# Performance work log

Hardware: AMD Instinct MI355X
Metric: run time of the kernel (lower is better)

## Reference

```python
import jax, jax.numpy as jnp
import numpy as np

FP8_MAX = 448.0  # e4m3fn max
ACT_EPS = 1e-4
W_EPS = 1e-6
BLK = 128


def quant_dequant_act_1x128(x):
    # x: [E, M, K]. One scale per (row, 128-col) tile; scale = max(|x|, eps)/448.
    E, M, K = x.shape
    xb = x.reshape(E, M, K // BLK, BLK)
    amax = jnp.max(jnp.abs(xb), axis=-1, keepdims=True)
    safe = jnp.maximum(amax, ACT_EPS)
    q = (xb * (FP8_MAX / safe)).astype(jnp.float8_e4m3fn)
    return (q.astype(jnp.float32) * (safe / FP8_MAX)).reshape(E, M, K)


def quant_dequant_weight_128x128(w):
    # w: [E, N, K]. One scale per 128x128 block; scale = max(|w|, eps)/448.
    E, N, K = w.shape
    wb = w.reshape(E, N // BLK, BLK, K // BLK, BLK)
    amax = jnp.max(jnp.abs(wb), axis=(2, 4), keepdims=True)
    safe = jnp.maximum(amax, W_EPS)
    q = (wb * (FP8_MAX / safe)).astype(jnp.float8_e4m3fn)
    return (q.astype(jnp.float32) * (safe / FP8_MAX)).reshape(E, N, K)


def setup_inputs() -> dict:
    key = jax.random.key(0)
    kx, kw = jax.random.split(key)
    E, M, K, N = 8, 4096, 2048, 2048
    x = jax.random.normal(kx, (E, M, K), dtype=jnp.float32)
    weight = jax.random.normal(kw, (E, N, K), dtype=jnp.float32) * 0.02
    return {"x": x, "weight": weight}


def reference(x, weight):
    # fp8 blockwise quantize both operands, then grouped GEMM per expert.
    xq = quant_dequant_act_1x128(x)          # [E, M, K]
    wq = quant_dequant_weight_128x128(weight)  # [E, N, K]
    return jnp.einsum('emk,enk->emn', xq, wq)  # [E, M, N]
```

## Files before the change

### kernel.cpp

```cpp
#include <hip/hip_runtime.h>

typedef float f32x4 __attribute__((ext_vector_type(4)));
typedef float f32x16 __attribute__((ext_vector_type(16)));

static constexpr int E_ = 8, M_ = 4096, K_ = 2048, N_ = 2048;
static constexpr int KB_ = 16;
static constexpr int NB128 = N_ / 128;
static constexpr int BM = 256, BN = 128, BK = 128;
static constexpr int KT = K_ / BK;
static constexpr int MT2 = M_ / BM;
static constexpr int NT2 = N_ / BN;
#define FP8MAX 448.0f

__global__ __launch_bounds__(256) void quant_x_kernel(const float* __restrict__ x,
                                                      unsigned char* __restrict__ qx,
                                                      float* __restrict__ sx) {
  long tile = (long)blockIdx.x * 8 + (threadIdx.x >> 5);
  int lane = threadIdx.x & 31;
  f32x4 v = *(const f32x4*)(x + tile * 128 + lane * 4);
  float am = fmaxf(fmaxf(fabsf(v[0]), fabsf(v[1])), fmaxf(fabsf(v[2]), fabsf(v[3])));
#pragma unroll
  for (int off = 16; off; off >>= 1) am = fmaxf(am, __shfl_xor(am, off, 32));
  float safe = fmaxf(am, 1e-4f);
  float qs = FP8MAX / safe;
  int pk = 0;
  pk = __builtin_amdgcn_cvt_pk_fp8_f32(v[0] * qs, v[1] * qs, pk, false);
  pk = __builtin_amdgcn_cvt_pk_fp8_f32(v[2] * qs, v[3] * qs, pk, true);
  *(int*)(qx + tile * 128 + lane * 4) = pk;
  if (lane == 0) sx[tile] = safe / FP8MAX;
}

__global__ __launch_bounds__(256) void quant_w_kernel(const float* __restrict__ w,
                                                      unsigned char* __restrict__ qw,
                                                      float* __restrict__ sw) {
  int b = blockIdx.x;
  int kb = b % KB_;
  int t2 = b / KB_;
  int nb = t2 % NB128;
  int e = t2 / NB128;
  int tid = threadIdx.x;
  int r = tid >> 1;
  int c0 = (tid & 1) * 64;
  const float* base = w + ((long)(e * N_ + nb * 128 + r)) * K_ + kb * 128 + c0;
  f32x4 v[16];
  float am = 0.f;
#pragma unroll
  for (int j = 0; j < 16; ++j) {
    v[j] = *(const f32x4*)(base + j * 4);
    am = fmaxf(am, fmaxf(fmaxf(fabsf(v[j][0]), fabsf(v[j][1])),
                         fmaxf(fabsf(v[j][2]), fabsf(v[j][3]))));
  }
#pragma unroll
  for (int off = 32; off; off >>= 1) am = fmaxf(am, __shfl_xor(am, off, 64));
  __shared__ float red[4];
  if ((tid & 63) == 0) red[tid >> 6] = am;
  __syncthreads();
  am = fmaxf(fmaxf(red[0], red[1]), fmaxf(red[2], red[3]));
  float safe = fmaxf(am, 1e-6f);
  float qs = FP8MAX / safe;
  unsigned char* outp = qw + ((long)(e * N_ + nb * 128 + r)) * K_ + kb * 128 + c0;
#pragma unroll
  for (int j4 = 0; j4 < 4; ++j4) {
    uint4 pkv;
    unsigned int* pp = (unsigned int*)&pkv;
#pragma unroll
    for (int q = 0; q < 4; ++q) {
      int j = j4 * 4 + q;
      int pk = 0;
      pk = __builtin_amdgcn_cvt_pk_fp8_f32(v[j][0] * qs, v[j][1] * qs, pk, false);
      pk = __builtin_amdgcn_cvt_pk_fp8_f32(v[j][2] * qs, v[j][3] * qs, pk, true);
      pp[q] = (unsigned int)pk;
    }
    *(uint4*)(outp + j4 * 16) = pkv;
  }
  if (tid == 0) sw[(e * NB128 + nb) * KB_ + kb] = safe / FP8MAX;
}

__device__ inline void gload16(const void* g, void* l) {
  __builtin_amdgcn_global_load_lds(
      (const __attribute__((address_space(1))) unsigned int*)g,
      (__attribute__((address_space(3))) unsigned int*)l, 16, 0, 0);
}

#define BAR __builtin_amdgcn_s_barrier()

#define MMACC(ACC, AV, BV, SXV)                                                 \
  do {                                                                          \
    f32x16 p = {0.f, 0.f, 0.f, 0.f, 0.f, 0.f, 0.f, 0.f,                        \
                0.f, 0.f, 0.f, 0.f, 0.f, 0.f, 0.f, 0.f};                        \
    __builtin_amdgcn_s_setprio(1);                                              \
    _Pragma("unroll") for (int ks = 0; ks < 8; ++ks)                            \
        p = __builtin_amdgcn_mfma_f32_32x32x16_fp8_fp8(AV[ks], BV[ks], p, 0, 0, 0); \
    __builtin_amdgcn_s_setprio(0);                                              \
    ACC += p * (SXV);                                                           \
  } while (0)

#define LDSX(SV, MB)                                                            \
  do {                                                                          \
    _Pragma("unroll") for (int g = 0; g < 4; ++g) {                             \
      f32x4 t = *(const f32x4*)&sxl[kt][wr * 64 + (MB) * 32 + hi * 4 + g * 8];  \
      _Pragma("unroll") for (int j = 0; j < 4; ++j) SV[g * 4 + j] = t[j] * swk; \
    }                                                                           \
  } while (0)

__global__ __launch_bounds__(512, 2) void gemm_kernel(
    const unsigned char* __restrict__ qx, const unsigned char* __restrict__ qw,
    const float* __restrict__ sx, const float* __restrict__ sw,
    float* __restrict__ out) {
  __shared__ unsigned char As[2][BM * BK];
  __shared__ unsigned char Bs[2][BN * BK];
  __shared__ float sxl[KT][BM];
  __shared__ float swl[KT];

  const int e = blockIdx.y;
  const int x = blockIdx.x;
  const int swz = (x & 7) * 32 + (x >> 3);
  const int mt = swz >> 4, nt = swz & 15;
  const int brow = mt * BM, bcol = nt * BN;

  const int tid = threadIdx.x;
  const int w = tid >> 6, l = tid & 63;
  const int wr = w >> 1, wc = w & 1;
  const int r32 = l & 31, hi = l >> 5, rx = l & 7;

  const unsigned char* Ab = qx + (size_t)(e * M_ + brow) * K_;
  const unsigned char* Bb = qw + (size_t)(e * N_ + bcol) * K_;

  {
    int row = tid >> 1, h = (tid & 1) * 8;
    const float* sp = sx + (size_t)(e * M_ + brow + row) * KB_ + h;
    f32x4 s0 = *(const f32x4*)sp;
    f32x4 s1 = *(const f32x4*)(sp + 4);
#pragma unroll
    for (int j = 0; j < 4; ++j) {
      sxl[h + j][row] = s0[j];
      sxl[h + 4 + j][row] = s1[j];
    }
    if (tid < KT) swl[tid] = sw[(e * NB128 + nt) * KB_ + tid];
  }
  __syncthreads();

  const int c8 = l & 7, r8 = (l >> 3) & 7;
  const int srcswz = (c8 ^ r8) * 16;
  auto stageA = [&](int rowbase, int kt2, int tb) {
    gload16(Ab + (size_t)(rowbase + w * 8 + (l >> 3)) * K_ + kt2 * BK + srcswz,
            &As[tb][(rowbase + w * 8) * BK]);
  };
  auto stageB = [&](int rowbase, int kt2, int tb) {
    gload16(Bb + (size_t)(rowbase + w * 8 + (l >> 3)) * K_ + kt2 * BK + srcswz,
            &Bs[tb][(rowbase + w * 8) * BK]);
  };

#pragma unroll
  for (int t = 0; t < 2; ++t) {
    stageA(0, t, t); stageA(64, t, t); stageA(128, t, t); stageA(192, t, t);
    stageB(0, t, t); stageB(64, t, t);
  }
  asm volatile("s_waitcnt vmcnt(6)" ::: "memory");
  BAR;
  __builtin_amdgcn_sched_barrier(0);

  f32x16 acc00 = {0.f}, acc01 = {0.f}, acc10 = {0.f}, acc11 = {0.f};
  int cofs[8];
#pragma unroll
  for (int ks = 0; ks < 8; ++ks) cofs[ks] = ((ks ^ rx) * 16) + hi * 8;
  const int arow_b = (wr * 64 + r32) * BK;
  const int brow_b = (wc * 64 + r32) * BK;

  long a0[8], a1[8], b0[8], b1[8];
  f32x16 sx0, sx1;

  for (int kt = 0; kt < KT; ++kt) {
    const int buf = kt & 1;
    const unsigned char* Acur = As[buf];
    const unsigned char* Bcur = Bs[buf];
    const float swk = swl[kt];

    LDSX(sx0, 0);
#pragma unroll
    for (int ks = 0; ks < 8; ++ks) a0[ks] = *(const long*)&Acur[arow_b + cofs[ks]];
#pragma unroll
    for (int ks = 0; ks < 8; ++ks) b0[ks] = *(const long*)&Bcur[brow_b + cofs[ks]];
    BAR;
    MMACC(acc00, a0, b0, sx0);
    BAR;
#pragma unroll
    for (int ks = 0; ks < 8; ++ks)
      b1[ks] = *(const long*)&Bcur[brow_b + 32 * BK + cofs[ks]];
    BAR;
    MMACC(acc01, a0, b1, sx0);
    BAR;
    if (kt + 2 < KT) { stageB(0, kt + 2, buf); stageB(64, kt + 2, buf); }
#pragma unroll
    for (int ks = 0; ks < 8; ++ks)
      a1[ks] = *(const long*)&Acur[arow_b + 32 * BK + cofs[ks]];
    LDSX(sx1, 1);
    BAR;
    MMACC(acc10, a1, b0, sx1);
    BAR;
    if (kt + 2 < KT) { stageA(0, kt + 2, buf); stageA(64, kt + 2, buf);
                       stageA(128, kt + 2, buf); stageA(192, kt + 2, buf); }
    BAR;
    MMACC(acc11, a1, b1, sx1);
    if (kt < KT - 2)       { asm volatile("s_waitcnt vmcnt(6)" ::: "memory"); }
    else if (kt == KT - 2) { asm volatile("s_waitcnt vmcnt(0)" ::: "memory"); }
    BAR;
    __builtin_amdgcn_sched_barrier(0);
  }

#pragma unroll
  for (int mb = 0; mb < 2; ++mb) {
#pragma unroll
    for (int nb = 0; nb < 2; ++nb) {
      const f32x16 accv = mb == 0 ? (nb == 0 ? acc00 : acc01)
                                  : (nb == 0 ? acc10 : acc11);
      const int n = bcol + wc * 64 + nb * 32 + r32;
#pragma unroll
      for (int r = 0; r < 16; ++r) {
        const int m = brow + wr * 64 + mb * 32 + (r & 3) + 8 * (r >> 2) + 4 * hi;
        out[(size_t)(e * M_ + m) * N_ + n] = accv[r];
      }
    }
  }
}

extern "C" void kernel_launch(void* const* d_in, const int* in_sizes, int n_in,
                              void* d_out, int out_size, void* d_ws, size_t ws_size,
                              hipStream_t stream) {
  const float* x = (const float*)d_in[0];
  const float* wt = (const float*)d_in[1];
  float* out = (float*)d_out;

  unsigned char* ws = (unsigned char*)d_ws;
  unsigned char* qx = ws;
  unsigned char* qw = ws + (size_t)E_ * M_ * K_;
  float* sx = (float*)(qw + (size_t)E_ * N_ * K_);
  float* sw = sx + (size_t)E_ * M_ * KB_;

  quant_x_kernel<<<dim3((E_ * M_ * KB_) / 8), dim3(256), 0, stream>>>(x, qx, sx);
  quant_w_kernel<<<dim3(E_ * NB128 * KB_), dim3(256), 0, stream>>>(wt, qw, sw);
  gemm_kernel<<<dim3(MT2 * NT2, E_), dim3(512), 0, stream>>>(qx, qw, sx, sw, out);
}
```

Baseline: 466.6 us.

## Enlarge GEMM block tile to 256x256 with 2x4 warp layout and 128x64 warp tiles

Doubles the GEMM block tile along N to 256, rearranging the 8 waves as 2x4 so each wave computes a 128x64 sub-tile with eight accumulators. Each A fragment read from LDS now feeds two MFMA chains, which raises arithmetic intensity per LDS and global byte and halves A re-reads across N tiles. The pipeline schedule is rewritten with more B staging per step, new wait counts, and weight scales stored per 128-column half. The cost is higher register pressure (eight f32x16 accumulators plus six fragment arrays) and more LDS (128KB double-buffered), which may cut occupancy below the declared 2 blocks per CU.

```diff
diff --git a/kernel.cpp b/kernel.cpp
--- a/kernel.cpp
+++ b/kernel.cpp
@@ -6,7 +6,7 @@
 static constexpr int E_ = 8, M_ = 4096, K_ = 2048, N_ = 2048;
 static constexpr int KB_ = 16;
 static constexpr int NB128 = N_ / 128;
-static constexpr int BM = 256, BN = 128, BK = 128;
+static constexpr int BM = 256, BN = 256, BK = 128;
 static constexpr int KT = K_ / BK;
 static constexpr int MT2 = M_ / BM;
 static constexpr int NT2 = N_ / BN;
@@ -84,21 +84,29 @@
 
 #define BAR __builtin_amdgcn_s_barrier()
 
-#define MMACC(ACC, AV, BV, SXV)                                                 \
+#define MM2(AV, ACC0, ACC1, SXV)                                                \
   do {                                                                          \
-    f32x16 p = {0.f, 0.f, 0.f, 0.f, 0.f, 0.f, 0.f, 0.f,                        \
-                0.f, 0.f, 0.f, 0.f, 0.f, 0.f, 0.f, 0.f};                        \
+    f32x16 p0 = {0.f, 0.f, 0.f, 0.f, 0.f, 0.f, 0.f, 0.f,                       \
+                 0.f, 0.f, 0.f, 0.f, 0.f, 0.f, 0.f, 0.f};                       \
+    f32x16 p1 = p0;                                                             \
     __builtin_amdgcn_s_setprio(1);                                              \
-    _Pragma("unroll") for (int ks = 0; ks < 8; ++ks)                            \
-        p = __builtin_amdgcn_mfma_f32_32x32x16_fp8_fp8(AV[ks], BV[ks], p, 0, 0, 0); \
+    _Pragma("unroll") for (int ks = 0; ks < 8; ++ks) {                          \
+      p0 = __builtin_amdgcn_mfma_f32_32x32x16_fp8_fp8(AV[ks], b0[ks], p0, 0, 0, 0); \
+      p1 = __builtin_amdgcn_mfma_f32_32x32x16_fp8_fp8(AV[ks], b1[ks], p1, 0, 0, 0); \
+    }                                                                           \
     __builtin_amdgcn_s_setprio(0);                                              \
-    ACC += p * (SXV);                                                           \
+    ACC0 += p0 * (SXV);                                                         \
+    ACC1 += p1 * (SXV);                                                         \
   } while (0)
+
+#define RD8(DST, BASE, ROFF)                                                    \
+  _Pragma("unroll") for (int ks = 0; ks < 8; ++ks)                              \
+      DST[ks] = *(const long*)&(BASE)[(ROFF) + cofs[ks]];
 
 #define LDSX(SV, MB)                                                            \
   do {                                                                          \
     _Pragma("unroll") for (int g = 0; g < 4; ++g) {                             \
-      f32x4 t = *(const f32x4*)&sxl[kt][wr * 64 + (MB) * 32 + hi * 4 + g * 8];  \
+      f32x4 t = *(const f32x4*)&sxl[kt][wr * 128 + (MB) * 32 + hi * 4 + g * 8]; \
       _Pragma("unroll") for (int j = 0; j < 4; ++j) SV[g * 4 + j] = t[j] * swk; \
     }                                                                           \
   } while (0)
@@ -110,17 +118,17 @@
   __shared__ unsigned char As[2][BM * BK];
   __shared__ unsigned char Bs[2][BN * BK];
   __shared__ float sxl[KT][BM];
-  __shared__ float swl[KT];
+  __shared__ float swl[2][KT];
 
   const int e = blockIdx.y;
   const int x = blockIdx.x;
-  const int swz = (x & 7) * 32 + (x >> 3);
-  const int mt = swz >> 4, nt = swz & 15;
+  const int swz = (x & 7) * 16 + (x >> 3);
+  const int mt = swz >> 3, nt = swz & 7;
   const int brow = mt * BM, bcol = nt * BN;
 
   const int tid = threadIdx.x;
   const int w = tid >> 6, l = tid & 63;
-  const int wr = w >> 1, wc = w & 1;
+  const int wr = w >> 2, wc = w & 3;
   const int r32 = l & 31, hi = l >> 5, rx = l & 7;
 
   const unsigned char* Ab = qx + (size_t)(e * M_ + brow) * K_;
@@ -136,12 +144,12 @@
       sxl[h + j][row] = s0[j];
       sxl[h + 4 + j][row] = s1[j];
     }
-    if (tid < KT) swl[tid] = sw[(e * NB128 + nt) * KB_ + tid];
-  }
-  __syncthreads();
-
-  const int c8 = l & 7, r8 = (l >> 3) & 7;
-  const int srcswz = (c8 ^ r8) * 16;
+    if (tid < 32)
+      swl[tid >> 4][tid & 15] =
+          sw[(e * NB128 + nt * 2 + (tid >> 4)) * KB_ + (tid & 15)];
+  }
+
+  const int srcswz = ((l & 7) ^ ((l >> 3) & 7)) * 16;
   auto stageA = [&](int rowbase, int kt2, int tb) {
     gload16(Ab + (size_t)(rowbase + w * 8 + (l >> 3)) * K_ + kt2 * BK + srcswz,
             &As[tb][(rowbase + w * 8) * BK]);
@@ -154,70 +162,80 @@
 #pragma unroll
   for (int t = 0; t < 2; ++t) {
     stageA(0, t, t); stageA(64, t, t); stageA(128, t, t); stageA(192, t, t);
-    stageB(0, t, t); stageB(64, t, t);
-  }
-  asm volatile("s_waitcnt vmcnt(6)" ::: "memory");
+    stageB(0, t, t); stageB(64, t, t); stageB(128, t, t); stageB(192, t, t);
+  }
+  asm volatile("s_waitcnt vmcnt(8) lgkmcnt(0)" ::: "memory");
   BAR;
   __builtin_amdgcn_sched_barrier(0);
 
   f32x16 acc00 = {0.f}, acc01 = {0.f}, acc10 = {0.f}, acc11 = {0.f};
+  f32x16 acc20 = {0.f}, acc21 = {0.f}, acc30 = {0.f}, acc31 = {0.f};
   int cofs[8];
 #pragma unroll
   for (int ks = 0; ks < 8; ++ks) cofs[ks] = ((ks ^ rx) * 16) + hi * 8;
-  const int arow_b = (wr * 64 + r32) * BK;
-  const int brow_b = (wc * 64 + r32) * BK;
-
-  long a0[8], a1[8], b0[8], b1[8];
-  f32x16 sx0, sx1;
+  const int arow0 = (wr * 128 + r32) * BK;
+  const int brow0 = (wc * 64 + r32) * BK;
+
+  long a0[8], a1[8], a2[8], a3[8], b0[8], b1[8];
+  f32x16 sx0, sx1, sx2, sx3;
 
   for (int kt = 0; kt < KT; ++kt) {
     const int buf = kt & 1;
     const unsigned char* Acur = As[buf];
     const unsigned char* Bcur = Bs[buf];
-    const float swk = swl[kt];
+    const float swk = swl[wc >> 1][kt];
 
     LDSX(sx0, 0);
-#pragma unroll
-    for (int ks = 0; ks < 8; ++ks) a0[ks] = *(const long*)&Acur[arow_b + cofs[ks]];
-#pragma unroll
-    for (int ks = 0; ks < 8; ++ks) b0[ks] = *(const long*)&Bcur[brow_b + cofs[ks]];
-    BAR;
-    MMACC(acc00, a0, b0, sx0);
-    BAR;
-#pragma unroll
-    for (int ks = 0; ks < 8; ++ks)
-      b1[ks] = *(const long*)&Bcur[brow_b + 32 * BK + cofs[ks]];
-    BAR;
-    MMACC(acc01, a0, b1, sx0);
-    BAR;
-    if (kt + 2 < KT) { stageB(0, kt + 2, buf); stageB(64, kt + 2, buf); }
-#pragma unroll
-    for (int ks = 0; ks < 8; ++ks)
-      a1[ks] = *(const long*)&Acur[arow_b + 32 * BK + cofs[ks]];
+    RD8(a0, Acur, arow0);
+    RD8(b0, Bcur, brow0);
+    RD8(b1, Bcur, brow0 + 32 * BK);
+    BAR;
+    MM2(a0, acc00, acc01, sx0);
+    BAR;
     LDSX(sx1, 1);
-    BAR;
-    MMACC(acc10, a1, b0, sx1);
-    BAR;
+    RD8(a1, Acur, arow0 + 32 * BK);
+    RD8(a2, Acur, arow0 + 64 * BK);
+    if (kt + 2 < KT) { stageB(0, kt + 2, buf); stageB(64, kt + 2, buf);
+                       stageB(128, kt + 2, buf); stageB(192, kt + 2, buf); }
+    BAR;
+    MM2(a1, acc10, acc11, sx1);
+    BAR;
+    LDSX(sx2, 2);
+    RD8(a3, Acur, arow0 + 96 * BK);
+    BAR;
+    MM2(a2, acc20, acc21, sx2);
+    BAR;
+    LDSX(sx3, 3);
+    asm volatile("s_waitcnt lgkmcnt(0)" ::: "memory");
+    BAR;
+    __builtin_amdgcn_sched_barrier(0);
     if (kt + 2 < KT) { stageA(0, kt + 2, buf); stageA(64, kt + 2, buf);
                        stageA(128, kt + 2, buf); stageA(192, kt + 2, buf); }
-    BAR;
-    MMACC(acc11, a1, b1, sx1);
-    if (kt < KT - 2)       { asm volatile("s_waitcnt vmcnt(6)" ::: "memory"); }
-    else if (kt == KT - 2) { asm volatile("s_waitcnt vmcnt(0)" ::: "memory"); }
-    BAR;
-    __builtin_amdgcn_sched_barrier(0);
-  }
-
-#pragma unroll
-  for (int mb = 0; mb < 2; ++mb) {
+    MM2(a3, acc30, acc31, sx3);
+    if (kt < KT - 2) {
+      asm volatile("s_waitcnt vmcnt(8)" ::: "memory");
+      BAR;
+      __builtin_amdgcn_sched_barrier(0);
+    } else if (kt == KT - 2) {
+      asm volatile("s_waitcnt vmcnt(0)" ::: "memory");
+      BAR;
+      __builtin_amdgcn_sched_barrier(0);
+    }
+  }
+
+#pragma unroll
+  for (int mb = 0; mb < 4; ++mb) {
 #pragma unroll
     for (int nb = 0; nb < 2; ++nb) {
-      const f32x16 accv = mb == 0 ? (nb == 0 ? acc00 : acc01)
-                                  : (nb == 0 ? acc10 : acc11);
+      const f32x16 accv =
+          mb == 0 ? (nb == 0 ? acc00 : acc01)
+        : mb == 1 ? (nb == 0 ? acc10 : acc11)
+        : mb == 2 ? (nb == 0 ? acc20 : acc21)
+                  : (nb == 0 ? acc30 : acc31);
       const int n = bcol + wc * 64 + nb * 32 + r32;
 #pragma unroll
       for (int r = 0; r < 16; ++r) {
-        const int m = brow + wr * 64 + mb * 32 + (r & 3) + 8 * (r >> 2) + 4 * hi;
+        const int m = brow + wr * 128 + mb * 32 + (r & 3) + 8 * (r >> 2) + 4 * hi;
         out[(size_t)(e * M_ + m) * N_ + n] = accv[r];
       }
     }
```

Result: slower. 1.701 ms (+264.5%).
